# Kernel optimization log

Measured on AMD Instinct MI355X. Metric: run time of the kernel, lower is better.

## Reference

```python
import jax, jax.numpy as jnp
import numpy as np

L, H, P = 32768, 256, 256
DT_MIN, DT_MAX = 0.001, 0.1


def setup_inputs() -> dict:
    key = jax.random.key(0)
    ks = jax.random.split(key, 7)
    signal = jax.random.normal(ks[0], (L, H), jnp.float32)
    # stable HiPPO-like init: negative real part, random imaginary part
    lam_re = -(0.1 + 0.4 * jax.random.uniform(ks[1], (P,), jnp.float32))
    lam_im = jax.random.normal(ks[2], (P,), jnp.float32)
    Lambda_ri = jnp.stack([lam_re, lam_im], axis=-1)            # (P, 2)
    B_ri = jax.random.normal(ks[3], (P, H, 2), jnp.float32) / np.float32(np.sqrt(H))
    C_ri = jax.random.normal(ks[4], (H, P, 2), jnp.float32) / np.float32(np.sqrt(P))
    D = jax.random.uniform(ks[5], (H,), jnp.float32)
    log_step = jnp.log(DT_MIN + (DT_MAX - DT_MIN) * jax.random.uniform(ks[6], (P,), jnp.float32))
    return {"signal": signal, "Lambda_ri": Lambda_ri, "B_ri": B_ri,
            "C_ri": C_ri, "D": D, "log_step": log_step}


def reference(signal, Lambda_ri, B_ri, C_ri, D, log_step):
    # --- get_BC_tilde (bcInit='dense'): B stored real (P,H,2) -> complex ---
    Lambda = jax.lax.complex(Lambda_ri[..., 0], Lambda_ri[..., 1])   # (P,)
    B_tilde = jax.lax.complex(B_ri[..., 0], B_ri[..., 1])            # (P, H)
    C_tilde = jax.lax.complex(C_ri[..., 0], C_ri[..., 1])            # (H, P)

    # --- discretize_zoh ---
    step = jnp.exp(log_step)                                          # (P,) step_scale = 1.0
    Lambda_bar = jnp.exp(Lambda * step)                               # (P,) complex
    B_bar = ((Lambda_bar - 1.0) / Lambda)[:, None] * B_tilde          # (P, H) complex

    # --- apply_ssm: Bu_elements = vmap(u -> B_bar @ u) over time ---
    Bu = signal.astype(Lambda_bar.dtype) @ B_bar.T                    # (L, P) complex
    Lam = jnp.broadcast_to(Lambda_bar, Bu.shape)                      # (L, P)

    def binop(qi, qj):
        A_i, Bu_i = qi
        A_j, Bu_j = qj
        return (A_j * A_i, Bu_j + A_j * Bu_i)

    _, xs = jax.lax.associative_scan(binop, (Lam, Bu), axis=0)        # (L, P)

    # y = Re(C_tilde @ x) + D * u, vectorized over time
    y = jnp.real(xs @ C_tilde.T) + D * signal                         # (L, H)
    return y
```

## Files before the change

kernel.cpp:

```cpp
#include <hip/hip_runtime.h>
#include <math.h>

constexpr int L = 32768;
constexpr int H = 256;
constexpr int P = 256;
constexpr int T = 64;
constexpr int NC = L / T;
constexpr int N1 = 2 * P;
constexpr int LDA = 40;
constexpr int LDEP = 130;

typedef __attribute__((ext_vector_type(8))) short short8;
typedef __attribute__((ext_vector_type(4))) float f32x4;

__device__ __forceinline__ unsigned f2bf(float f) {
  unsigned u = __float_as_uint(f);
  return (u + 0x7FFFu + ((u >> 16) & 1u)) >> 16;
}
__device__ __forceinline__ float bf_lo(unsigned u) { return __uint_as_float(u << 16); }
__device__ __forceinline__ float bf_hi(unsigned u) { return __uint_as_float(u & 0xFFFF0000u); }

__device__ __forceinline__ void gload_lds16(const unsigned short* g, unsigned short* l) {
  __builtin_amdgcn_global_load_lds(
      (const __attribute__((address_space(1))) unsigned int*)(g),
      (__attribute__((address_space(3))) unsigned int*)(l), 16, 0, 0);
}

__device__ __forceinline__ void lambda_bar_of(const float* __restrict__ lam,
                                              const float* __restrict__ lstep,
                                              int p, float& lbr, float& lbi) {
  float lr = lam[2 * p], li = lam[2 * p + 1];
  float st = expf(lstep[p]);
  float ea = expf(lr * st);
  lbr = ea * cosf(li * st);
  lbi = ea * sinf(li * st);
}

__global__ __launch_bounds__(256) void k_prep(const float* __restrict__ lam,
                                              const float* __restrict__ lstep,
                                              const float* __restrict__ Bri,
                                              const float* __restrict__ Cri,
                                              unsigned short* __restrict__ Bcat,
                                              unsigned short* __restrict__ Ccat,
                                              float* __restrict__ powr,
                                              float* __restrict__ powi) {
  int idx = blockIdx.x * 256 + threadIdx.x;
  if (idx < N1 * H) {
    int n = idx >> 8, k = idx & 255;
    int p = n >> 1, comp = n & 1;
    float lr = lam[2 * p], li = lam[2 * p + 1];
    float st = expf(lstep[p]);
    float ea = expf(lr * st);
    float lbr = ea * cosf(li * st), lbi = ea * sinf(li * st);
    float inv = 1.0f / (lr * lr + li * li);
    float nr = lbr - 1.0f;
    float fr = (nr * lr + lbi * li) * inv;
    float fi = (lbi * lr - nr * li) * inv;
    float br = Bri[2 * (p * H + k)], bi = Bri[2 * (p * H + k) + 1];
    float v = (comp == 0) ? (fr * br - fi * bi) : (fr * bi + fi * br);
    Bcat[idx] = (unsigned short)f2bf(v);
  } else if (idx < 2 * N1 * H) {
    int j = idx - N1 * H;
    int h = j >> 9, k2 = j & 511;
    int p = k2 >> 1;
    float v = ((k2 & 1) == 0) ? Cri[2 * (h * P + p)] : -Cri[2 * (h * P + p) + 1];
    Ccat[j] = (unsigned short)f2bf(v);
  } else {
    int r = idx - 2 * N1 * H;
    int t = r >> 8, p = r & 255;
    float lr = lam[2 * p], li = lam[2 * p + 1];
    float st = expf(lstep[p]);
    float e = (float)(t + 1);
    float er = expf(e * lr * st);
    powr[r] = er * cosf(e * li * st);
    powi[r] = er * sinf(e * li * st);
  }
}

__global__ __launch_bounds__(256) void k_gemm1s(const float* __restrict__ sig,
                                                const unsigned short* __restrict__ Bcat,
                                                const float* __restrict__ lam,
                                                const float* __restrict__ lstep,
                                                unsigned short* __restrict__ Xl,
                                                float* __restrict__ Sr,
                                                float* __restrict__ Si) {
  constexpr int K = 256, NIT = K / 32;
  __shared__ __align__(16) char smem[36864];
  unsigned short* sA[2] = {(unsigned short*)smem, (unsigned short*)smem + 5120};
  unsigned short* sB[2] = {(unsigned short*)smem + 10240, (unsigned short*)smem + 14336};
  float* sEpi = (float*)smem;
  const int tid = threadIdx.x;
  const int lane = tid & 63;
  const int wave = tid >> 6;
  const int wr = (wave >> 1) * 64, wc = (wave & 1) * 64;
  const int m0 = blockIdx.x * 128, n0 = blockIdx.y * 128;
  const int ar = tid >> 1, aq = (tid & 1) * 16;
  const int br = tid >> 2, bq = (tid & 3) * 8;
  const int frow = lane & 15, fk = (lane >> 4) * 8;
  f32x4 acc[4][4];
#pragma unroll
  for (int i = 0; i < 4; i++)
#pragma unroll
    for (int j = 0; j < 4; j++) acc[i][j] = (f32x4){0.f, 0.f, 0.f, 0.f};

  float4 aR[4];
  const float* abase = sig + (size_t)(m0 + ar) * K + aq;
#define LOAD_A(k0) { const float* s_ = abase + (k0); \
    aR[0] = *(const float4*)(s_); aR[1] = *(const float4*)(s_ + 4); \
    aR[2] = *(const float4*)(s_ + 8); aR[3] = *(const float4*)(s_ + 12); }
#define WRITE_A(buf) { uint4 w0, w1; \
    w0.x = f2bf(aR[0].x) | (f2bf(aR[0].y) << 16); w0.y = f2bf(aR[0].z) | (f2bf(aR[0].w) << 16); \
    w0.z = f2bf(aR[1].x) | (f2bf(aR[1].y) << 16); w0.w = f2bf(aR[1].z) | (f2bf(aR[1].w) << 16); \
    w1.x = f2bf(aR[2].x) | (f2bf(aR[2].y) << 16); w1.y = f2bf(aR[2].z) | (f2bf(aR[2].w) << 16); \
    w1.z = f2bf(aR[3].x) | (f2bf(aR[3].y) << 16); w1.w = f2bf(aR[3].z) | (f2bf(aR[3].w) << 16); \
    *(uint4*)(sA[buf] + ar * LDA + aq) = w0; *(uint4*)(sA[buf] + ar * LDA + aq + 8) = w1; }
#define ISSUE_B(k0, buf) { \
    gload_lds16(Bcat + (size_t)(n0 + br) * K + (k0) + bq, sB[buf] + tid * 8); \
    gload_lds16(Bcat + (size_t)(n0 + 64 + br) * K + (k0) + bq, sB[buf] + 2048 + tid * 8); }

  LOAD_A(0);
  ISSUE_B(0, 0);
  WRITE_A(0);
  LOAD_A(32);
  __syncthreads();
#pragma unroll
  for (int it = 0; it < NIT; it++) {
    const int cur = it & 1, nxt = cur ^ 1;
    if (it + 1 < NIT) {
      WRITE_A(nxt);
      ISSUE_B((it + 1) * 32, nxt);
      if (it + 2 < NIT) LOAD_A((it + 2) * 32);
    }
    short8 af[4], bf[4];
#pragma unroll
    for (int i = 0; i < 4; i++) af[i] = *(const short8*)(sA[cur] + (wr + i * 16 + frow) * LDA + fk);
#pragma unroll
    for (int j = 0; j < 4; j++) bf[j] = *(const short8*)(sB[cur] + (wc + j * 16 + frow) * 32 + fk);
#pragma unroll
    for (int i = 0; i < 4; i++)
#pragma unroll
      for (int j = 0; j < 4; j++)
        acc[i][j] = __builtin_amdgcn_mfma_f32_16x16x32_bf16(af[i], bf[j], acc[i][j], 0, 0, 0);
    __syncthreads();
  }

  const int crow = (lane >> 4) * 4, ccol = wc + (lane & 15);
#pragma unroll
  for (int half = 0; half < 2; half++) {
    if ((wave >> 1) == half) {
#pragma unroll
      for (int i = 0; i < 4; i++)
#pragma unroll
        for (int j = 0; j < 4; j++)
#pragma unroll
          for (int g = 0; g < 4; g++)
            sEpi[(crow + i * 16 + g) * LDEP + ccol + j * 16] = acc[i][j][g];
    }
    __syncthreads();
    if (tid < 64) {
      const int pl = tid;
      const int gp = (n0 >> 1) + pl;
      const int c = blockIdx.x * 2 + half;
      float lbr, lbi;
      lambda_bar_of(lam, lstep, gp, lbr, lbi);
      float xr = 0.f, xi = 0.f;
      const float* e = sEpi + 2 * pl;
      const size_t gbase = (size_t)(m0 + half * 64) * N1 + n0 + 2 * pl;
      for (int tb = 0; tb < T; tb += 8) {
        float2 v[8];
#pragma unroll
        for (int u = 0; u < 8; u++) v[u] = *(const float2*)(e + (tb + u) * LDEP);
        unsigned ov[8];
#pragma unroll
        for (int u = 0; u < 8; u++) {
          float nr = fmaf(lbr, xr, fmaf(-lbi, xi, v[u].x));
          float ni = fmaf(lbr, xi, fmaf(lbi, xr, v[u].y));
          xr = nr; xi = ni;
          ov[u] = f2bf(xr) | (f2bf(xi) << 16);
        }
#pragma unroll
        for (int u = 0; u < 8; u++)
          *(unsigned*)(Xl + gbase + (size_t)(tb + u) * N1) = ov[u];
      }
      Sr[c * P + gp] = xr;
      Si[c * P + gp] = xi;
    }
    __syncthreads();
  }
#undef LOAD_A
#undef WRITE_A
#undef ISSUE_B
}

__global__ __launch_bounds__(64) void k_carry2(const float* __restrict__ lam,
                                               const float* __restrict__ lstep,
                                               const float* __restrict__ Sr,
                                               const float* __restrict__ Si,
                                               float* __restrict__ car, float* __restrict__ cai) {
  const int p = blockIdx.x;
  const int t = threadIdx.x;
  float lr = lam[2 * p], li = lam[2 * p + 1];
  float st = expf(lstep[p]);
  float eT = expf((float)T * lr * st);
  float lTr = eT * cosf((float)T * li * st);
  float lTi = eT * sinf((float)T * li * st);
  float vr[8], vi[8];
#pragma unroll
  for (int u = 0; u < 8; u++) {
    vr[u] = Sr[(t * 8 + u) * P + p];
    vi[u] = Si[(t * 8 + u) * P + p];
  }
  float Br = 0.f, Bi = 0.f;
#pragma unroll
  for (int u = 0; u < 8; u++) {
    float nr = fmaf(lTr, Br, fmaf(-lTi, Bi, vr[u]));
    float ni = fmaf(lTr, Bi, fmaf(lTi, Br, vi[u]));
    Br = nr; Bi = ni;
  }
  float e8 = expf(8.0f * (float)T * lr * st);
  float Ar = e8 * cosf(8.0f * (float)T * li * st);
  float Ai = e8 * sinf(8.0f * (float)T * li * st);
#pragma unroll
  for (int d = 1; d < 64; d <<= 1) {
    float Aor = __shfl_up(Ar, d), Aoi = __shfl_up(Ai, d);
    float Bor = __shfl_up(Br, d), Boi = __shfl_up(Bi, d);
    if (t >= d) {
      float nBr = Ar * Bor - Ai * Boi + Br;
      float nBi = Ar * Boi + Ai * Bor + Bi;
      float nAr = Aor * Ar - Aoi * Ai;
      float nAi = Aor * Ai + Aoi * Ar;
      Br = nBr; Bi = nBi; Ar = nAr; Ai = nAi;
    }
  }
  float cr = __shfl_up(Br, 1), ci = __shfl_up(Bi, 1);
  if (t == 0) { cr = 0.f; ci = 0.f; }
#pragma unroll
  for (int u = 0; u < 8; u++) {
    car[(t * 8 + u) * P + p] = cr;
    cai[(t * 8 + u) * P + p] = ci;
    float nr = fmaf(lTr, cr, fmaf(-lTi, ci, vr[u]));
    float ni = fmaf(lTr, ci, fmaf(lTi, cr, vi[u]));
    cr = nr; ci = ni;
  }
}

__global__ __launch_bounds__(256) void k_gemm2f(const unsigned short* __restrict__ Xl,
                                                const unsigned short* __restrict__ Ccat,
                                                const float* __restrict__ powr,
                                                const float* __restrict__ powi,
                                                const float* __restrict__ car,
                                                const float* __restrict__ cai,
                                                const float* __restrict__ sig,
                                                const float* __restrict__ Dv,
                                                float* __restrict__ out) {
  constexpr int K = 512, NIT = K / 32;
  __shared__ __align__(16) char smem[36864];
  unsigned short* sA[2] = {(unsigned short*)smem, (unsigned short*)smem + 5120};
  unsigned short* sB[2] = {(unsigned short*)smem + 10240, (unsigned short*)smem + 14336};
  const int tid = threadIdx.x;
  const int lane = tid & 63;
  const int wave = tid >> 6;
  const int wr = (wave >> 1) * 64, wc = (wave & 1) * 64;
  const int m0 = blockIdx.x * 128, n0 = blockIdx.y * 128;
  const int ar = tid >> 1, aq = (tid & 1) * 16;
  const int t_ = ar & 63;
  const int cc = blockIdx.x * 2 + (ar >> 6);
  const int br = tid >> 2, bq = (tid & 3) * 8;
  const int frow = lane & 15, fk = (lane >> 4) * 8;
  f32x4 acc[4][4];
#pragma unroll
  for (int i = 0; i < 4; i++)
#pragma unroll
    for (int j = 0; j < 4; j++) acc[i][j] = (f32x4){0.f, 0.f, 0.f, 0.f};

  uint4 x0, x1;
  float4 pr0, pr1, pi0, pi1, cr0, cr1, ci0, ci1;
  const unsigned short* xbase = Xl + (size_t)(m0 + ar) * N1 + aq;
  const float* prb = powr + t_ * P;
  const float* pib = powi + t_ * P;
  const float* crb = car + cc * P;
  const float* cib = cai + cc * P;
#define LOAD_A2(k0) { int p0_ = ((k0) >> 1) + (tid & 1) * 8; \
    x0 = *(const uint4*)(xbase + (k0)); x1 = *(const uint4*)(xbase + (k0) + 8); \
    pr0 = *(const float4*)(prb + p0_); pr1 = *(const float4*)(prb + p0_ + 4); \
    pi0 = *(const float4*)(pib + p0_); pi1 = *(const float4*)(pib + p0_ + 4); \
    cr0 = *(const float4*)(crb + p0_); cr1 = *(const float4*)(crb + p0_ + 4); \
    ci0 = *(const float4*)(cib + p0_); ci1 = *(const float4*)(cib + p0_ + 4); }
#define WRITE_A2(buf) { \
    unsigned xw[8] = {x0.x, x0.y, x0.z, x0.w, x1.x, x1.y, x1.z, x1.w}; \
    float pr_[8] = {pr0.x, pr0.y, pr0.z, pr0.w, pr1.x, pr1.y, pr1.z, pr1.w}; \
    float pi_[8] = {pi0.x, pi0.y, pi0.z, pi0.w, pi1.x, pi1.y, pi1.z, pi1.w}; \
    float cr_[8] = {cr0.x, cr0.y, cr0.z, cr0.w, cr1.x, cr1.y, cr1.z, cr1.w}; \
    float ci_[8] = {ci0.x, ci0.y, ci0.z, ci0.w, ci1.x, ci1.y, ci1.z, ci1.w}; \
    unsigned wo[8]; \
    _Pragma("unroll") for (int j_ = 0; j_ < 8; j_++) { \
      float xgr = bf_lo(xw[j_]) + (pr_[j_] * cr_[j_] - pi_[j_] * ci_[j_]); \
      float xgi = bf_hi(xw[j_]) + (pr_[j_] * ci_[j_] + pi_[j_] * cr_[j_]); \
      wo[j_] = f2bf(xgr) | (f2bf(xgi) << 16); } \
    uint4 w0, w1; \
    w0.x = wo[0]; w0.y = wo[1]; w0.z = wo[2]; w0.w = wo[3]; \
    w1.x = wo[4]; w1.y = wo[5]; w1.z = wo[6]; w1.w = wo[7]; \
    *(uint4*)(sA[buf] + ar * LDA + aq) = w0; *(uint4*)(sA[buf] + ar * LDA + aq + 8) = w1; }
#define ISSUE_B2(k0, buf) { \
    gload_lds16(Ccat + (size_t)(n0 + br) * K + (k0) + bq, sB[buf] + tid * 8); \
    gload_lds16(Ccat + (size_t)(n0 + 64 + br) * K + (k0) + bq, sB[buf] + 2048 + tid * 8); }

  LOAD_A2(0);
  ISSUE_B2(0, 0);
  WRITE_A2(0);
  LOAD_A2(32);
  __syncthreads();
#pragma unroll
  for (int it = 0; it < NIT; it++) {
    const int cur = it & 1, nxt = cur ^ 1;
    if (it + 1 < NIT) {
      WRITE_A2(nxt);
      ISSUE_B2((it + 1) * 32, nxt);
      if (it + 2 < NIT) LOAD_A2((it + 2) * 32);
    }
    short8 af[4], bf[4];
#pragma unroll
    for (int i = 0; i < 4; i++) af[i] = *(const short8*)(sA[cur] + (wr + i * 16 + frow) * LDA + fk);
#pragma unroll
    for (int j = 0; j < 4; j++) bf[j] = *(const short8*)(sB[cur] + (wc + j * 16 + frow) * 32 + fk);
#pragma unroll
    for (int i = 0; i < 4; i++)
#pragma unroll
      for (int j = 0; j < 4; j++)
        acc[i][j] = __builtin_amdgcn_mfma_f32_16x16x32_bf16(af[i], bf[j], acc[i][j], 0, 0, 0);
    __syncthreads();
  }

  const int crow = wr + (lane >> 4) * 4, ccol = wc + (lane & 15);
  float dcol[4];
#pragma unroll
  for (int j = 0; j < 4; j++) dcol[j] = Dv[n0 + ccol + j * 16];
#pragma unroll
  for (int i = 0; i < 4; i++)
#pragma unroll
    for (int j = 0; j < 4; j++) {
      int col = n0 + ccol + j * 16;
#pragma unroll
      for (int g = 0; g < 4; g++) {
        int row = m0 + crow + i * 16 + g;
        out[(size_t)row * H + col] = acc[i][j][g] + dcol[j] * sig[(size_t)row * H + col];
      }
    }
#undef LOAD_A2
#undef WRITE_A2
#undef ISSUE_B2
}

extern "C" void kernel_launch(void* const* d_in, const int* in_sizes, int n_in,
                              void* d_out, int out_size, void* d_ws, size_t ws_size,
                              hipStream_t stream) {
  const float* sig = (const float*)d_in[0];
  const float* lam = (const float*)d_in[1];
  const float* Bri = (const float*)d_in[2];
  const float* Cri = (const float*)d_in[3];
  const float* Dv  = (const float*)d_in[4];
  const float* lst = (const float*)d_in[5];
  float* out = (float*)d_out;

  unsigned short* Bcat = (unsigned short*)d_ws;
  unsigned short* Ccat = Bcat + (size_t)N1 * H;
  unsigned short* Xl   = Ccat + (size_t)H * N1;
  float* powr = (float*)(Xl + (size_t)L * N1);
  float* powi = powr + T * P;
  float* Sr   = powi + T * P;
  float* Si   = Sr + NC * P;
  float* car  = Si + NC * P;
  float* cai  = car + NC * P;

  k_prep<<<(2 * N1 * H + T * P) / 256, 256, 0, stream>>>(lam, lst, Bri, Cri,
                                                         Bcat, Ccat, powr, powi);
  dim3 g1(L / 128, N1 / 128);
  k_gemm1s<<<g1, 256, 0, stream>>>(sig, Bcat, lam, lst, Xl, Sr, Si);
  k_carry2<<<NC / 2, 64, 0, stream>>>(lam, lst, Sr, Si, car, cai);
  dim3 g2(L / 128, H / 128);
  k_gemm2f<<<g2, 256, 0, stream>>>(Xl, Ccat, powr, powi, car, cai, sig, Dv, out);
}
```

Baseline: 153.8 us.

## Pre-convert signal to bf16 and load MFMA fragments directly from global memory

Result: slower. 223.1 us (+45.1%).

```diff
diff --git a/kernel.cpp b/kernel.cpp
--- a/kernel.cpp
+++ b/kernel.cpp
@@ -7,11 +7,11 @@
 constexpr int T = 64;
 constexpr int NC = L / T;
 constexpr int N1 = 2 * P;
-constexpr int LDA = 40;
 constexpr int LDEP = 130;
 
 typedef __attribute__((ext_vector_type(8))) short short8;
 typedef __attribute__((ext_vector_type(4))) float f32x4;
+typedef union { short8 s; uint4 u; } s8u4;
 
 __device__ __forceinline__ unsigned f2bf(float f) {
   unsigned u = __float_as_uint(f);
@@ -19,12 +19,6 @@
 }
 __device__ __forceinline__ float bf_lo(unsigned u) { return __uint_as_float(u << 16); }
 __device__ __forceinline__ float bf_hi(unsigned u) { return __uint_as_float(u & 0xFFFF0000u); }
-
-__device__ __forceinline__ void gload_lds16(const unsigned short* g, unsigned short* l) {
-  __builtin_amdgcn_global_load_lds(
-      (const __attribute__((address_space(1))) unsigned int*)(g),
-      (__attribute__((address_space(3))) unsigned int*)(l), 16, 0, 0);
-}
 
 __device__ __forceinline__ void lambda_bar_of(const float* __restrict__ lam,
                                               const float* __restrict__ lstep,
@@ -36,15 +30,30 @@
   lbi = ea * sinf(li * st);
 }
 
-__global__ __launch_bounds__(256) void k_prep(const float* __restrict__ lam,
-                                              const float* __restrict__ lstep,
-                                              const float* __restrict__ Bri,
-                                              const float* __restrict__ Cri,
-                                              unsigned short* __restrict__ Bcat,
-                                              unsigned short* __restrict__ Ccat,
-                                              float* __restrict__ powr,
-                                              float* __restrict__ powi) {
-  int idx = blockIdx.x * 256 + threadIdx.x;
+__global__ __launch_bounds__(256) void k_prep2(const float* __restrict__ sig,
+                                               const float* __restrict__ lam,
+                                               const float* __restrict__ lstep,
+                                               const float* __restrict__ Bri,
+                                               const float* __restrict__ Cri,
+                                               unsigned short* __restrict__ sigbf,
+                                               unsigned short* __restrict__ Bcat,
+                                               unsigned short* __restrict__ Ccat,
+                                               float* __restrict__ powr,
+                                               float* __restrict__ powi) {
+  const int bx = blockIdx.x;
+  if (bx < 4096) {
+    int i = bx * 256 + threadIdx.x;
+    const float4* ip = (const float4*)sig;
+    float4 a = ip[2 * i], b = ip[2 * i + 1];
+    uint4 o;
+    o.x = f2bf(a.x) | (f2bf(a.y) << 16);
+    o.y = f2bf(a.z) | (f2bf(a.w) << 16);
+    o.z = f2bf(b.x) | (f2bf(b.y) << 16);
+    o.w = f2bf(b.z) | (f2bf(b.w) << 16);
+    ((uint4*)sigbf)[i] = o;
+    return;
+  }
+  int idx = (bx - 4096) * 256 + threadIdx.x;
   if (idx < N1 * H) {
     int n = idx >> 8, k = idx & 255;
     int p = n >> 1, comp = n & 1;
@@ -77,119 +86,82 @@
   }
 }
 
-__global__ __launch_bounds__(256) void k_gemm1s(const float* __restrict__ sig,
-                                                const unsigned short* __restrict__ Bcat,
-                                                const float* __restrict__ lam,
-                                                const float* __restrict__ lstep,
-                                                unsigned short* __restrict__ Xl,
-                                                float* __restrict__ Sr,
-                                                float* __restrict__ Si) {
-  constexpr int K = 256, NIT = K / 32;
-  __shared__ __align__(16) char smem[36864];
-  unsigned short* sA[2] = {(unsigned short*)smem, (unsigned short*)smem + 5120};
-  unsigned short* sB[2] = {(unsigned short*)smem + 10240, (unsigned short*)smem + 14336};
-  float* sEpi = (float*)smem;
+__global__ __launch_bounds__(256) void k_gemm1(const unsigned short* __restrict__ sigbf,
+                                               const unsigned short* __restrict__ Bcat,
+                                               const float* __restrict__ lam,
+                                               const float* __restrict__ lstep,
+                                               unsigned short* __restrict__ Xl,
+                                               float* __restrict__ Sr,
+                                               float* __restrict__ Si) {
+  constexpr int K = 256;
+  __shared__ __align__(16) float sEpi[T * LDEP];
   const int tid = threadIdx.x;
   const int lane = tid & 63;
   const int wave = tid >> 6;
-  const int wr = (wave >> 1) * 64, wc = (wave & 1) * 64;
-  const int m0 = blockIdx.x * 128, n0 = blockIdx.y * 128;
-  const int ar = tid >> 1, aq = (tid & 1) * 16;
-  const int br = tid >> 2, bq = (tid & 3) * 8;
-  const int frow = lane & 15, fk = (lane >> 4) * 8;
-  f32x4 acc[4][4];
-#pragma unroll
-  for (int i = 0; i < 4; i++)
+  const int wr = (wave & 1) * 32, wc = (wave >> 1) * 64;
+  const int c = blockIdx.y;
+  const int m0 = c * 64;
+  const int n0 = blockIdx.x * 128;
+  const int frow = lane & 15, fko = (lane >> 4) * 8;
+  const unsigned short* Ab = sigbf + (size_t)(m0 + wr + frow) * H + fko;
+  const unsigned short* Bb = Bcat + (size_t)(n0 + wc + frow) * K + fko;
+  f32x4 acc[2][4];
+#pragma unroll
+  for (int i = 0; i < 2; i++)
 #pragma unroll
     for (int j = 0; j < 4; j++) acc[i][j] = (f32x4){0.f, 0.f, 0.f, 0.f};
 
-  float4 aR[4];
-  const float* abase = sig + (size_t)(m0 + ar) * K + aq;
-#define LOAD_A(k0) { const float* s_ = abase + (k0); \
-    aR[0] = *(const float4*)(s_); aR[1] = *(const float4*)(s_ + 4); \
-    aR[2] = *(const float4*)(s_ + 8); aR[3] = *(const float4*)(s_ + 12); }
-#define WRITE_A(buf) { uint4 w0, w1; \
-    w0.x = f2bf(aR[0].x) | (f2bf(aR[0].y) << 16); w0.y = f2bf(aR[0].z) | (f2bf(aR[0].w) << 16); \
-    w0.z = f2bf(aR[1].x) | (f2bf(aR[1].y) << 16); w0.w = f2bf(aR[1].z) | (f2bf(aR[1].w) << 16); \
-    w1.x = f2bf(aR[2].x) | (f2bf(aR[2].y) << 16); w1.y = f2bf(aR[2].z) | (f2bf(aR[2].w) << 16); \
-    w1.z = f2bf(aR[3].x) | (f2bf(aR[3].y) << 16); w1.w = f2bf(aR[3].z) | (f2bf(aR[3].w) << 16); \
-    *(uint4*)(sA[buf] + ar * LDA + aq) = w0; *(uint4*)(sA[buf] + ar * LDA + aq + 8) = w1; }
-#define ISSUE_B(k0, buf) { \
-    gload_lds16(Bcat + (size_t)(n0 + br) * K + (k0) + bq, sB[buf] + tid * 8); \
-    gload_lds16(Bcat + (size_t)(n0 + 64 + br) * K + (k0) + bq, sB[buf] + 2048 + tid * 8); }
-
-  LOAD_A(0);
-  ISSUE_B(0, 0);
-  WRITE_A(0);
-  LOAD_A(32);
-  __syncthreads();
-#pragma unroll
-  for (int it = 0; it < NIT; it++) {
-    const int cur = it & 1, nxt = cur ^ 1;
-    if (it + 1 < NIT) {
-      WRITE_A(nxt);
-      ISSUE_B((it + 1) * 32, nxt);
-      if (it + 2 < NIT) LOAD_A((it + 2) * 32);
-    }
-    short8 af[4], bf[4];
-#pragma unroll
-    for (int i = 0; i < 4; i++) af[i] = *(const short8*)(sA[cur] + (wr + i * 16 + frow) * LDA + fk);
-#pragma unroll
-    for (int j = 0; j < 4; j++) bf[j] = *(const short8*)(sB[cur] + (wc + j * 16 + frow) * 32 + fk);
-#pragma unroll
-    for (int i = 0; i < 4; i++)
+#pragma unroll
+  for (int k0 = 0; k0 < K; k0 += 32) {
+    short8 af[2], bf[4];
+    af[0] = *(const short8*)(Ab + k0);
+    af[1] = *(const short8*)(Ab + 16 * H + k0);
+#pragma unroll
+    for (int j = 0; j < 4; j++) bf[j] = *(const short8*)(Bb + j * 16 * K + k0);
+#pragma unroll
+    for (int i = 0; i < 2; i++)
 #pragma unroll
       for (int j = 0; j < 4; j++)
         acc[i][j] = __builtin_amdgcn_mfma_f32_16x16x32_bf16(af[i], bf[j], acc[i][j], 0, 0, 0);
-    __syncthreads();
   }
 
   const int crow = (lane >> 4) * 4, ccol = wc + (lane & 15);
 #pragma unroll
-  for (int half = 0; half < 2; half++) {
-    if ((wave >> 1) == half) {
-#pragma unroll
-      for (int i = 0; i < 4; i++)
-#pragma unroll
-        for (int j = 0; j < 4; j++)
-#pragma unroll
-          for (int g = 0; g < 4; g++)
-            sEpi[(crow + i * 16 + g) * LDEP + ccol + j * 16] = acc[i][j][g];
-    }
-    __syncthreads();
-    if (tid < 64) {
-      const int pl = tid;
-      const int gp = (n0 >> 1) + pl;
-      const int c = blockIdx.x * 2 + half;
-      float lbr, lbi;
-      lambda_bar_of(lam, lstep, gp, lbr, lbi);
-      float xr = 0.f, xi = 0.f;
-      const float* e = sEpi + 2 * pl;
-      const size_t gbase = (size_t)(m0 + half * 64) * N1 + n0 + 2 * pl;
-      for (int tb = 0; tb < T; tb += 8) {
-        float2 v[8];
-#pragma unroll
-        for (int u = 0; u < 8; u++) v[u] = *(const float2*)(e + (tb + u) * LDEP);
-        unsigned ov[8];
-#pragma unroll
-        for (int u = 0; u < 8; u++) {
-          float nr = fmaf(lbr, xr, fmaf(-lbi, xi, v[u].x));
-          float ni = fmaf(lbr, xi, fmaf(lbi, xr, v[u].y));
-          xr = nr; xi = ni;
-          ov[u] = f2bf(xr) | (f2bf(xi) << 16);
-        }
-#pragma unroll
-        for (int u = 0; u < 8; u++)
-          *(unsigned*)(Xl + gbase + (size_t)(tb + u) * N1) = ov[u];
+  for (int i = 0; i < 2; i++)
+#pragma unroll
+    for (int j = 0; j < 4; j++)
+#pragma unroll
+      for (int g = 0; g < 4; g++)
+        sEpi[(wr + i * 16 + crow + g) * LDEP + ccol + j * 16] = acc[i][j][g];
+  __syncthreads();
+
+  if (tid < 64) {
+    const int pl = tid;
+    const int gp = (n0 >> 1) + pl;
+    float lbr, lbi;
+    lambda_bar_of(lam, lstep, gp, lbr, lbi);
+    float xr = 0.f, xi = 0.f;
+    const float* e = sEpi + 2 * pl;
+    const size_t gbase = (size_t)m0 * N1 + n0 + 2 * pl;
+    for (int tb = 0; tb < T; tb += 8) {
+      float2 v[8];
+#pragma unroll
+      for (int u = 0; u < 8; u++) v[u] = *(const float2*)(e + (tb + u) * LDEP);
+      unsigned ov[8];
+#pragma unroll
+      for (int u = 0; u < 8; u++) {
+        float nr = fmaf(lbr, xr, fmaf(-lbi, xi, v[u].x));
+        float ni = fmaf(lbr, xi, fmaf(lbi, xr, v[u].y));
+        xr = nr; xi = ni;
+        ov[u] = f2bf(xr) | (f2bf(xi) << 16);
       }
-      Sr[c * P + gp] = xr;
-      Si[c * P + gp] = xi;
-    }
-    __syncthreads();
-  }
-#undef LOAD_A
-#undef WRITE_A
-#undef ISSUE_B
+#pragma unroll
+      for (int u = 0; u < 8; u++)
+        *(unsigned*)(Xl + gbase + (size_t)(tb + u) * N1) = ov[u];
+    }
+    Sr[c * P + gp] = xr;
+    Si[c * P + gp] = xi;
+  }
 }
 
 __global__ __launch_bounds__(64) void k_carry2(const float* __restrict__ lam,
@@ -244,111 +216,102 @@
   }
 }
 
-__global__ __launch_bounds__(256) void k_gemm2f(const unsigned short* __restrict__ Xl,
-                                                const unsigned short* __restrict__ Ccat,
-                                                const float* __restrict__ powr,
-                                                const float* __restrict__ powi,
-                                                const float* __restrict__ car,
-                                                const float* __restrict__ cai,
-                                                const float* __restrict__ sig,
-                                                const float* __restrict__ Dv,
-                                                float* __restrict__ out) {
-  constexpr int K = 512, NIT = K / 32;
-  __shared__ __align__(16) char smem[36864];
-  unsigned short* sA[2] = {(unsigned short*)smem, (unsigned short*)smem + 5120};
-  unsigned short* sB[2] = {(unsigned short*)smem + 10240, (unsigned short*)smem + 14336};
+__global__ __launch_bounds__(256) void k_gemm2(const unsigned short* __restrict__ Xl,
+                                               const unsigned short* __restrict__ Ccat,
+                                               const float* __restrict__ powr,
+                                               const float* __restrict__ powi,
+                                               const float* __restrict__ car,
+                                               const float* __restrict__ cai,
+                                               const unsigned short* __restrict__ sigbf,
+                                               const float* __restrict__ Dv,
+                                               float* __restrict__ out) {
+  constexpr int K = 512;
   const int tid = threadIdx.x;
   const int lane = tid & 63;
   const int wave = tid >> 6;
-  const int wr = (wave >> 1) * 64, wc = (wave & 1) * 64;
-  const int m0 = blockIdx.x * 128, n0 = blockIdx.y * 128;
-  const int ar = tid >> 1, aq = (tid & 1) * 16;
-  const int t_ = ar & 63;
-  const int cc = blockIdx.x * 2 + (ar >> 6);
-  const int br = tid >> 2, bq = (tid & 3) * 8;
-  const int frow = lane & 15, fk = (lane >> 4) * 8;
-  f32x4 acc[4][4];
-#pragma unroll
-  for (int i = 0; i < 4; i++)
+  const int wr = (wave & 1) * 32, wc = (wave >> 1) * 64;
+  const int c = blockIdx.y;
+  const int m0 = c * 64;
+  const int n0 = blockIdx.x * 128;
+  const int frow = lane & 15, fko = (lane >> 4) * 8;
+  const int pq = (lane >> 4) * 4;
+  const unsigned short* Ab = Xl + (size_t)(m0 + wr + frow) * N1 + fko;
+  const unsigned short* Bb = Ccat + (size_t)(n0 + wc + frow) * K + fko;
+  const float* pw0r = powr + (wr + frow) * P;
+  const float* pw0i = powi + (wr + frow) * P;
+  const float* pw1r = powr + (wr + 16 + frow) * P;
+  const float* pw1i = powi + (wr + 16 + frow) * P;
+  const float* crb = car + c * P;
+  const float* cib = cai + c * P;
+  f32x4 acc[2][4];
+#pragma unroll
+  for (int i = 0; i < 2; i++)
 #pragma unroll
     for (int j = 0; j < 4; j++) acc[i][j] = (f32x4){0.f, 0.f, 0.f, 0.f};
 
-  uint4 x0, x1;
-  float4 pr0, pr1, pi0, pi1, cr0, cr1, ci0, ci1;
-  const unsigned short* xbase = Xl + (size_t)(m0 + ar) * N1 + aq;
-  const float* prb = powr + t_ * P;
-  const float* pib = powi + t_ * P;
-  const float* crb = car + cc * P;
-  const float* cib = cai + cc * P;
-#define LOAD_A2(k0) { int p0_ = ((k0) >> 1) + (tid & 1) * 8; \
-    x0 = *(const uint4*)(xbase + (k0)); x1 = *(const uint4*)(xbase + (k0) + 8); \
-    pr0 = *(const float4*)(prb + p0_); pr1 = *(const float4*)(prb + p0_ + 4); \
-    pi0 = *(const float4*)(pib + p0_); pi1 = *(const float4*)(pib + p0_ + 4); \
-    cr0 = *(const float4*)(crb + p0_); cr1 = *(const float4*)(crb + p0_ + 4); \
-    ci0 = *(const float4*)(cib + p0_); ci1 = *(const float4*)(cib + p0_ + 4); }
-#define WRITE_A2(buf) { \
-    unsigned xw[8] = {x0.x, x0.y, x0.z, x0.w, x1.x, x1.y, x1.z, x1.w}; \
-    float pr_[8] = {pr0.x, pr0.y, pr0.z, pr0.w, pr1.x, pr1.y, pr1.z, pr1.w}; \
-    float pi_[8] = {pi0.x, pi0.y, pi0.z, pi0.w, pi1.x, pi1.y, pi1.z, pi1.w}; \
-    float cr_[8] = {cr0.x, cr0.y, cr0.z, cr0.w, cr1.x, cr1.y, cr1.z, cr1.w}; \
-    float ci_[8] = {ci0.x, ci0.y, ci0.z, ci0.w, ci1.x, ci1.y, ci1.z, ci1.w}; \
-    unsigned wo[8]; \
-    _Pragma("unroll") for (int j_ = 0; j_ < 8; j_++) { \
-      float xgr = bf_lo(xw[j_]) + (pr_[j_] * cr_[j_] - pi_[j_] * ci_[j_]); \
-      float xgi = bf_hi(xw[j_]) + (pr_[j_] * ci_[j_] + pi_[j_] * cr_[j_]); \
-      wo[j_] = f2bf(xgr) | (f2bf(xgi) << 16); } \
-    uint4 w0, w1; \
-    w0.x = wo[0]; w0.y = wo[1]; w0.z = wo[2]; w0.w = wo[3]; \
-    w1.x = wo[4]; w1.y = wo[5]; w1.z = wo[6]; w1.w = wo[7]; \
-    *(uint4*)(sA[buf] + ar * LDA + aq) = w0; *(uint4*)(sA[buf] + ar * LDA + aq + 8) = w1; }
-#define ISSUE_B2(k0, buf) { \
-    gload_lds16(Ccat + (size_t)(n0 + br) * K + (k0) + bq, sB[buf] + tid * 8); \
-    gload_lds16(Ccat + (size_t)(n0 + 64 + br) * K + (k0) + bq, sB[buf] + 2048 + tid * 8); }
-
-  LOAD_A2(0);
-  ISSUE_B2(0, 0);
-  WRITE_A2(0);
-  LOAD_A2(32);
-  __syncthreads();
-#pragma unroll
-  for (int it = 0; it < NIT; it++) {
-    const int cur = it & 1, nxt = cur ^ 1;
-    if (it + 1 < NIT) {
-      WRITE_A2(nxt);
-      ISSUE_B2((it + 1) * 32, nxt);
-      if (it + 2 < NIT) LOAD_A2((it + 2) * 32);
-    }
-    short8 af[4], bf[4];
-#pragma unroll
-    for (int i = 0; i < 4; i++) af[i] = *(const short8*)(sA[cur] + (wr + i * 16 + frow) * LDA + fk);
-#pragma unroll
-    for (int j = 0; j < 4; j++) bf[j] = *(const short8*)(sB[cur] + (wc + j * 16 + frow) * 32 + fk);
-#pragma unroll
-    for (int i = 0; i < 4; i++)
-#pragma unroll
-      for (int j = 0; j < 4; j++)
-        acc[i][j] = __builtin_amdgcn_mfma_f32_16x16x32_bf16(af[i], bf[j], acc[i][j], 0, 0, 0);
-    __syncthreads();
-  }
-
-  const int crow = wr + (lane >> 4) * 4, ccol = wc + (lane & 15);
+#pragma unroll 4
+  for (int k0 = 0; k0 < K; k0 += 32) {
+    const int p0 = (k0 >> 1) + pq;
+    uint4 x0 = *(const uint4*)(Ab + k0);
+    uint4 x1 = *(const uint4*)(Ab + 16 * N1 + k0);
+    float4 a0r = *(const float4*)(pw0r + p0), a0i = *(const float4*)(pw0i + p0);
+    float4 a1r = *(const float4*)(pw1r + p0), a1i = *(const float4*)(pw1i + p0);
+    float4 g4r = *(const float4*)(crb + p0), g4i = *(const float4*)(cib + p0);
+    float grv[4] = {g4r.x, g4r.y, g4r.z, g4r.w};
+    float giv[4] = {g4i.x, g4i.y, g4i.z, g4i.w};
+    s8u4 A0, A1;
+    {
+      unsigned xw[4] = {x0.x, x0.y, x0.z, x0.w};
+      float pr[4] = {a0r.x, a0r.y, a0r.z, a0r.w};
+      float pi_[4] = {a0i.x, a0i.y, a0i.z, a0i.w};
+      unsigned wo[4];
+#pragma unroll
+      for (int j = 0; j < 4; j++) {
+        float xgr = fmaf(pr[j], grv[j], fmaf(-pi_[j], giv[j], bf_lo(xw[j])));
+        float xgi = fmaf(pr[j], giv[j], fmaf(pi_[j], grv[j], bf_hi(xw[j])));
+        wo[j] = f2bf(xgr) | (f2bf(xgi) << 16);
+      }
+      A0.u.x = wo[0]; A0.u.y = wo[1]; A0.u.z = wo[2]; A0.u.w = wo[3];
+    }
+    {
+      unsigned xw[4] = {x1.x, x1.y, x1.z, x1.w};
+      float pr[4] = {a1r.x, a1r.y, a1r.z, a1r.w};
+      float pi_[4] = {a1i.x, a1i.y, a1i.z, a1i.w};
+      unsigned wo[4];
+#pragma unroll
+      for (int j = 0; j < 4; j++) {
+        float xgr = fmaf(pr[j], grv[j], fmaf(-pi_[j], giv[j], bf_lo(xw[j])));
+        float xgi = fmaf(pr[j], giv[j], fmaf(pi_[j], grv[j], bf_hi(xw[j])));
+        wo[j] = f2bf(xgr) | (f2bf(xgi) << 16);
+      }
+      A1.u.x = wo[0]; A1.u.y = wo[1]; A1.u.z = wo[2]; A1.u.w = wo[3];
+    }
+    short8 bf[4];
+#pragma unroll
+    for (int j = 0; j < 4; j++) bf[j] = *(const short8*)(Bb + j * 16 * K + k0);
+#pragma unroll
+    for (int j = 0; j < 4; j++) {
+      acc[0][j] = __builtin_amdgcn_mfma_f32_16x16x32_bf16(A0.s, bf[j], acc[0][j], 0, 0, 0);
+      acc[1][j] = __builtin_amdgcn_mfma_f32_16x16x32_bf16(A1.s, bf[j], acc[1][j], 0, 0, 0);
+    }
+  }
+
+  const int crow = (lane >> 4) * 4, ccol = wc + (lane & 15);
   float dcol[4];
 #pragma unroll
   for (int j = 0; j < 4; j++) dcol[j] = Dv[n0 + ccol + j * 16];
 #pragma unroll
-  for (int i = 0; i < 4; i++)
+  for (int i = 0; i < 2; i++)
 #pragma unroll
     for (int j = 0; j < 4; j++) {
       int col = n0 + ccol + j * 16;
 #pragma unroll
       for (int g = 0; g < 4; g++) {
-        int row = m0 + crow + i * 16 + g;
-        out[(size_t)row * H + col] = acc[i][j][g] + dcol[j] * sig[(size_t)row * H + col];
+        int row = m0 + wr + i * 16 + crow + g;
+        float sv = __uint_as_float((unsigned)sigbf[(size_t)row * H + col] << 16);
+        out[(size_t)row * H + col] = acc[i][j][g] + dcol[j] * sv;
       }
     }
-#undef LOAD_A2
-#undef WRITE_A2
-#undef ISSUE_B2
 }
 
 extern "C" void kernel_launch(void* const* d_in, const int* in_sizes, int n_in,
@@ -362,9 +325,10 @@
   const float* lst = (const float*)d_in[5];
   float* out = (float*)d_out;
 
-  unsigned short* Bcat = (unsigned short*)d_ws;
-  unsigned short* Ccat = Bcat + (size_t)N1 * H;
-  unsigned short* Xl   = Ccat + (size_t)H * N1;
+  unsigned short* sigbf = (unsigned short*)d_ws;
+  unsigned short* Bcat  = sigbf + (size_t)L * H;
+  unsigned short* Ccat  = Bcat + (size_t)N1 * H;
+  unsigned short* Xl    = Ccat + (size_t)H * N1;
   float* powr = (float*)(Xl + (size_t)L * N1);
   float* powi = powr + T * P;
   float* Sr   = powi + T * P;
@@ -372,11 +336,11 @@
   float* car  = Si + NC * P;
   float* cai  = car + NC * P;
 
-  k_prep<<<(2 * N1 * H + T * P) / 256, 256, 0, stream>>>(lam, lst, Bri, Cri,
-                                                         Bcat, Ccat, powr, powi);
-  dim3 g1(L / 128, N1 / 128);
-  k_gemm1s<<<g1, 256, 0, stream>>>(sig, Bcat, lam, lst, Xl, Sr, Si);
-  k_carry2<<<NC / 2, 64, 0, stream>>>(lam, lst, Sr, Si, car, cai);
-  dim3 g2(L / 128, H / 128);
-  k_gemm2f<<<g2, 256, 0, stream>>>(Xl, Ccat, powr, powi, car, cai, sig, Dv, out);
-}
+  k_prep2<<<4096 + 1088, 256, 0, stream>>>(sig, lam, lst, Bri, Cri,
+                                           sigbf, Bcat, Ccat, powr, powi);
+  dim3 g1(N1 / 128, NC);
+  k_gemm1<<<g1, 256, 0, stream>>>(sigbf, Bcat, lam, lst, Xl, Sr, Si);
+  k_carry2<<<P, 64, 0, stream>>>(lam, lst, Sr, Si, car, cai);
+  dim3 g2(H / 128, NC);
+  k_gemm2<<<g2, 256, 0, stream>>>(Xl, Ccat, powr, powi, car, cai, sigbf, Dv, out);
+}
```
